# Kernel tuning notes

Measured on AMD Instinct MI355X. Metric: run time of the kernel, lower is better.

Reference implementation:

```python
import jax, jax.numpy as jnp
import numpy as np

EPS = 1e-5
GROUPS = 32


def conv1x1(x, W, b):
    # x: (B,C,T), W: (O,C), b: (O,)
    return jnp.einsum('bct,oc->bot', x, W) + b[None, :, None]


def group_norm(x, gamma, beta):
    B, C, T = x.shape
    xg = x.reshape(B, GROUPS, (C // GROUPS) * T)
    mu = xg.mean(axis=-1, keepdims=True)
    var = xg.var(axis=-1, keepdims=True)
    xn = ((xg - mu) * jax.lax.rsqrt(var + EPS)).reshape(B, C, T)
    return xn * gamma[None, :, None] + beta[None, :, None]


def block(x, W, b, gamma, beta):
    return jax.nn.relu(group_norm(conv1x1(x, W, b), gamma, beta))


def setup_inputs() -> dict:
    key = jax.random.key(0)
    ks = jax.random.split(key, 8)
    B, C, P, T, TF = 4, 512, 512, 2048, 4096
    inp = {
        'feature': jax.random.normal(ks[0], (B, C, T), jnp.float32),
        'frame_level_feature': jax.random.uniform(ks[1], (B, C, TF), jnp.float32),
        # cur_point_conv: conv1x1 C->P + GN(32,P)
        'W1': jax.random.normal(ks[2], (P, C), jnp.float32) / np.sqrt(C),
        'b1': jnp.zeros((P,), jnp.float32),
        'g1': jnp.ones((P,), jnp.float32),
        'be1': jnp.zeros((P,), jnp.float32),
        # lr_conv: conv1x1 C->2P + GN(32,2P)
        'W2': jax.random.normal(ks[3], (2 * P, C), jnp.float32) / np.sqrt(C),
        'b2': jnp.zeros((2 * P,), jnp.float32),
        'g2': jnp.ones((2 * P,), jnp.float32),
        'be2': jnp.zeros((2 * P,), jnp.float32),
        # proposal_conv: conv1x1 4P->C + GN(32,C)
        'W3': jax.random.normal(ks[4], (C, 4 * P), jnp.float32) / np.sqrt(4 * P),
        'b3': jnp.zeros((C,), jnp.float32),
        'g3': jnp.ones((C,), jnp.float32),
        'be3': jnp.zeros((C,), jnp.float32),
    }
    return inp


def reference(feature, frame_level_feature, W1, b1, g1, be1, W2, b2, g2, be2, W3, b3, g3, be3):
    fm_short = block(feature, W1, b1, g1, be1)          # (B,P,T)
    feat = block(feature, W2, b2, g2, be2)              # (B,2P,T)
    t = feature.shape[2]
    # inverse-CDF resampling (uses batch 0 statistics, as original)
    mean_values = frame_level_feature.mean(axis=1)[0]   # (TF,)
    mean_values = mean_values / mean_values.sum()
    cdf = (jnp.cumsum(mean_values) * t).astype(jnp.int32)
    cdf = jnp.minimum(cdf, t - 1)                       # (TF,)
    # exact vectorization of findNearNum loop: first index with minimal |cdf-i|
    targets = jnp.arange(t, dtype=jnp.int32)
    idx = jnp.argmin(jnp.abs(cdf[None, :] - targets[:, None]), axis=1)  # (t,)
    sampled = frame_level_feature[:, :, idx]            # (B,C,t)
    mixed = jnp.concatenate([sampled, feat, fm_short], axis=1)  # (B,4P,t)
    mixed = block(mixed, W3, b3, g3, be3)               # (B,C,t)
    return (mixed, feat)
```

## Files before the change

### kernel.cpp

```cpp
#include <hip/hip_runtime.h>

typedef unsigned short u16;
typedef unsigned int   u32;
typedef __attribute__((ext_vector_type(8))) short short8;
typedef __attribute__((ext_vector_type(4))) float f32x4;

__device__ __forceinline__ float bf2f(u16 v) {
  return __uint_as_float(((u32)v) << 16);
}
__device__ __forceinline__ u16 f2bf(float f) {
  u32 u = __float_as_uint(f);
  u32 r = (u + 0x7FFFu + ((u >> 16) & 1u)) >> 16;
  return (u16)r;
}
__device__ __forceinline__ float relu(float x) { return x < 0.f ? 0.f : x; }

__device__ __forceinline__ void gld16(const void* g, void* l) {
  __builtin_amdgcn_global_load_lds((const __attribute__((address_space(1))) u32*)g,
                                   (__attribute__((address_space(3))) u32*)l, 16, 0, 0);
}

__global__ void colmean_part_kernel(const float* __restrict__ frame,
                                    double* __restrict__ partD) {
  int tf = blockIdx.x * 256 + threadIdx.x;
  int ch = blockIdx.y;
  const float* f0 = frame + tf + (size_t)ch * 64 * 4096;
  double s = 0.0;
  for (int c = 0; c < 64; ++c) s += (double)f0[(size_t)c * 4096];
  partD[ch * 4096 + tf] = s;
}

__global__ void scanD_kernel(const double* __restrict__ partD, int* __restrict__ cdf) {
  __shared__ double part[256];
  __shared__ double base[256];
  __shared__ double Ss;
  int tid = threadIdx.x;
  double loc[16];
  double s = 0.0;
#pragma unroll
  for (int i = 0; i < 16; ++i) {
    int tf = tid * 16 + i;
    double m = 0.0;
#pragma unroll
    for (int ch = 0; ch < 8; ++ch) m += partD[ch * 4096 + tf];
    loc[i] = m / 512.0;
    s += loc[i];
  }
  part[tid] = s;
  __syncthreads();
  if (tid == 0) {
    double t = 0.0;
    for (int i = 0; i < 256; ++i) t += part[i];
    Ss = t;
  }
  __syncthreads();
  double S = Ss;
  s = 0.0;
#pragma unroll
  for (int i = 0; i < 16; ++i) { loc[i] = loc[i] / S; s += loc[i]; }
  part[tid] = s;
  __syncthreads();
  if (tid == 0) {
    double c = 0.0;
    for (int i = 0; i < 256; ++i) { base[i] = c; c += part[i]; }
  }
  __syncthreads();
  double c = base[tid];
#pragma unroll
  for (int i = 0; i < 16; ++i) {
    c += loc[i];
    int iv = (int)(c * 2048.0);
    cdf[tid * 16 + i] = iv < 2047 ? iv : 2047;
  }
}

__global__ void argmin_kernel(const int* __restrict__ cdf, int* __restrict__ idx) {
  __shared__ int sd[256], sj[256];
  int target = blockIdx.x;
  int tid = threadIdx.x;
  int best = 0x7fffffff, bj = 0x7fffffff;
  for (int j = tid; j < 4096; j += 256) {
    int d = cdf[j] - target; d = d < 0 ? -d : d;
    if (d < best) { best = d; bj = j; }
  }
  sd[tid] = best; sj[tid] = bj;
  __syncthreads();
  for (int s = 128; s > 0; s >>= 1) {
    if (tid < s) {
      if (sd[tid+s] < sd[tid] || (sd[tid+s] == sd[tid] && sj[tid+s] < sj[tid])) {
        sd[tid] = sd[tid+s]; sj[tid] = sj[tid+s];
      }
    }
    __syncthreads();
  }
  if (tid == 0) idx[target] = sj[0];
}

__global__ void gatherT_kernel(const float* __restrict__ frame, const int* __restrict__ idx,
                               u16* __restrict__ X3T) {
  __shared__ u16 tile[64][65];
  __shared__ int sidx[64];
  int cb = blockIdx.x * 64, t0 = blockIdx.y * 64, b = blockIdx.z;
  int tid = threadIdx.x;
  if (tid < 64) {
    int it = idx[t0 + tid];
    sidx[tid] = it < 0 ? 0 : (it > 4095 ? 4095 : it);
  }
  __syncthreads();
  const float* fb = frame + (size_t)b * 512 * 4096;
  for (int i = tid; i < 4096; i += 256) {
    int r = i >> 6, tt = i & 63;
    tile[tt][r] = f2bf(fb[(size_t)(cb + r) * 4096 + sidx[tt]]);
  }
  __syncthreads();
  u16* xb = X3T + (size_t)b * 2048 * 2048;
  for (int i = tid; i < 4096; i += 256) {
    int r = i >> 6, cc = i & 63;
    xb[(size_t)(t0 + r) * 2048 + cb + cc] = tile[r][cc];
  }
}

__global__ void transposeCT_kernel(const float* __restrict__ X, u16* __restrict__ XT) {
  __shared__ u16 tile[64][65];
  int cb = blockIdx.x * 64, t0 = blockIdx.y * 64, b = blockIdx.z;
  int tid = threadIdx.x;
  const float* xb = X + (size_t)b * 512 * 2048;
  for (int i = tid; i < 4096; i += 256) {
    int r = i >> 6, tt = i & 63;
    tile[tt][r] = f2bf(xb[(size_t)(cb + r) * 2048 + t0 + tt]);
  }
  __syncthreads();
  u16* xtb = XT + (size_t)b * 2048 * 512;
  for (int i = tid; i < 4096; i += 256) {
    int r = i >> 6, cc = i & 63;
    xtb[(size_t)(t0 + r) * 512 + cb + cc] = tile[r][cc];
  }
}

__global__ void convW_kernel(const float* __restrict__ src, u16* __restrict__ dst, int n) {
  int i = blockIdx.x * 256 + threadIdx.x;
  if (i < n) dst[i] = f2bf(src[i]);
}

__global__ __launch_bounds__(128) void gemm_bt2(
    const u16* __restrict__ A, const u16* __restrict__ Bt,
    const float* __restrict__ bias, float* __restrict__ Y,
    int M, int N, int K)
{
  __shared__ short As[2][2048];
  __shared__ short Bs[2][4096];
  const int tid = threadIdx.x;
  const int lane = tid & 63;
  const int w = tid >> 6;
  const int nt = blockIdx.x, mt = blockIdx.y, bb = blockIdx.z;

  const u16* Ab = A + (size_t)mt * 64 * K;
  const u16* Bb = Bt + ((size_t)bb * N + (size_t)nt * 128) * K;

  const int lm = lane & 15, lq = lane >> 4;

  f32x4 acc[4][4] = {};
  const int nsteps = K >> 5;

  auto stage = [&](int buf, int kt) {
#pragma unroll
    for (int p = 0; p < 2; ++p) {
      int chunk = tid + 128 * p;
      int row = chunk >> 2, ko = (chunk & 3) << 3;
      gld16(Ab + (size_t)row * K + kt + ko, (char*)As[buf] + chunk * 16);
    }
#pragma unroll
    for (int p = 0; p < 4; ++p) {
      int chunk = tid + 128 * p;
      int row = chunk >> 2, ko = (chunk & 3) << 3;
      gld16(Bb + (size_t)row * K + kt + ko, (char*)Bs[buf] + chunk * 16);
    }
  };

  stage(0, 0);
  for (int s = 0; s < nsteps; ++s) {
    int cur = s & 1;
    __syncthreads();
    if (s + 1 < nsteps) stage(cur ^ 1, (s + 1) << 5);
    short8 af[4], bfv[4];
#pragma unroll
    for (int i = 0; i < 4; ++i)
      af[i] = *(const short8*)(As[cur] + ((i * 16 + lm) * 32 + lq * 8));
#pragma unroll
    for (int j = 0; j < 4; ++j)
      bfv[j] = *(const short8*)(Bs[cur] + ((w * 64 + j * 16 + lm) * 32 + lq * 8));
#pragma unroll
    for (int i = 0; i < 4; ++i)
#pragma unroll
      for (int j = 0; j < 4; ++j)
        acc[i][j] = __builtin_amdgcn_mfma_f32_16x16x32_bf16(af[i], bfv[j], acc[i][j], 0, 0, 0);
  }

#pragma unroll
  for (int i = 0; i < 4; ++i) {
    int mbase = mt * 64 + i * 16 + lq * 4;
#pragma unroll
    for (int e = 0; e < 4; ++e) {
      int m = mbase + e;
      float bv = bias[m];
      float* yp = Y + ((size_t)bb * M + m) * N + nt * 128 + w * 64 + lm;
#pragma unroll
      for (int j = 0; j < 4; ++j)
        yp[j * 16] = acc[i][j][e] + bv;
    }
  }
}

__global__ void stats_part_kernel(const float* __restrict__ Y, float* __restrict__ raw,
                                  int C, int cpg) {
  int chunk = blockIdx.x, g = blockIdx.y, b = blockIdx.z, tid = threadIdx.x;
  const float* base = Y + ((size_t)b * C + (size_t)g * cpg) * 2048 + (size_t)chunk * 4096;
  float s = 0.f, ss = 0.f;
#pragma unroll
  for (int i = 0; i < 16; ++i) {
    float v = base[tid + 256 * i];
    s += v; ss += v * v;
  }
  __shared__ float s1[256], s2[256];
  s1[tid] = s; s2[tid] = ss;
  __syncthreads();
  for (int st = 128; st > 0; st >>= 1) {
    if (tid < st) { s1[tid] += s1[tid + st]; s2[tid] += s2[tid + st]; }
    __syncthreads();
  }
  if (tid == 0) {
    atomicAdd(&raw[(b * 32 + g) * 2],     s1[0]);
    atomicAdd(&raw[(b * 32 + g) * 2 + 1], s2[0]);
  }
}

__global__ void stats_fin_kernel(const float* __restrict__ raw, float* __restrict__ stats,
                                 float n) {
  int i = threadIdx.x;
  float mu = raw[i * 2] / n;
  float var = raw[i * 2 + 1] / n - mu * mu;
  stats[i * 2] = mu;
  stats[i * 2 + 1] = 1.0f / sqrtf(var + 1e-5f);
}

__global__ void normT_kernel(const float* __restrict__ Y, const float* __restrict__ stats,
                             const float* __restrict__ gamma, const float* __restrict__ beta,
                             int C, int gShift, u16* __restrict__ X3T, int colBase,
                             float* __restrict__ featOut) {
  __shared__ u16 tile[64][65];
  int b = blockIdx.z, c0 = blockIdx.y * 64, t0 = blockIdx.x * 64;
  const float* yb = Y + (size_t)b * C * 2048;
  for (int i = threadIdx.x; i < 4096; i += 256) {
    int r = i >> 6, cc = i & 63;
    int ch = c0 + r;
    int gI = (b * 32 + (ch >> gShift)) * 2;
    float mu = stats[gI], rs = stats[gI + 1];
    float v = yb[(size_t)ch * 2048 + t0 + cc];
    float o = relu((v - mu) * rs * gamma[ch] + beta[ch]);
    tile[cc][r] = f2bf(o);
    if (featOut) featOut[((size_t)b * C + ch) * 2048 + t0 + cc] = o;
  }
  __syncthreads();
  for (int i = threadIdx.x; i < 4096; i += 256) {
    int r = i >> 6, cc = i & 63;
    X3T[((size_t)b * 2048 + t0 + r) * 2048 + colBase + c0 + cc] = tile[r][cc];
  }
}

__global__ void norm3_kernel(const float* __restrict__ Y, const float* __restrict__ stats,
                             const float* __restrict__ gamma, const float* __restrict__ beta,
                             float* __restrict__ out) {
  int i = blockIdx.x * 256 + threadIdx.x;
  int b = i >> 20;
  int ch = (i >> 11) & 511;
  int gI = (b * 32 + (ch >> 4)) * 2;
  float mu = stats[gI], rs = stats[gI + 1];
  out[i] = relu((Y[i] - mu) * rs * gamma[ch] + beta[ch]);
}

extern "C" void kernel_launch(void* const* d_in, const int* in_sizes, int n_in,
                              void* d_out, int out_size, void* d_ws, size_t ws_size,
                              hipStream_t stream) {
  const float* feature = (const float*)d_in[0];
  const float* frame   = (const float*)d_in[1];
  const float* W1 = (const float*)d_in[2];
  const float* b1 = (const float*)d_in[3];
  const float* g1 = (const float*)d_in[4];
  const float* be1 = (const float*)d_in[5];
  const float* W2 = (const float*)d_in[6];
  const float* b2 = (const float*)d_in[7];
  const float* g2 = (const float*)d_in[8];
  const float* be2 = (const float*)d_in[9];
  const float* W3 = (const float*)d_in[10];
  const float* b3 = (const float*)d_in[11];
  const float* g3 = (const float*)d_in[12];
  const float* be3 = (const float*)d_in[13];

  char* ws = (char*)d_ws;
  u16*    X3T   = (u16*)(ws + 0);
  float*  Y1f   = (float*)(ws + 33554432);
  float*  Y2f   = (float*)(ws + 50331648);
  float*  Y3f   = Y1f;
  u16*    featT = (u16*)(ws + 83886080);
  double* partD = (double*)(ws + 50331648);
  u16*    W1b   = (u16*)(ws + 50331648 + 1048576);
  u16*    W2b   = (u16*)(ws + 33554432);
  u16*    W3b   = (u16*)(ws + 50331648);
  int*    cdf   = (int*)(ws + 92307456);
  int*    idx   = (int*)(ws + 92323840);
  float*  raw1  = (float*)(ws + 92340224);
  float*  raw2  = (float*)(ws + 92341248);
  float*  raw3  = (float*)(ws + 92342272);
  float*  st1   = (float*)(ws + 92343296);
  float*  st2   = (float*)(ws + 92344320);
  float*  st3   = (float*)(ws + 92345344);

  float* outMixed = (float*)d_out;
  float* outFeat  = outMixed + (size_t)4 * 512 * 2048;

  hipMemsetAsync(raw1, 0, 3 * 1024, stream);

  colmean_part_kernel<<<dim3(16, 8), 256, 0, stream>>>(frame, partD);
  scanD_kernel<<<1, 256, 0, stream>>>(partD, cdf);
  argmin_kernel<<<2048, 256, 0, stream>>>(cdf, idx);
  gatherT_kernel<<<dim3(8, 32, 4), 256, 0, stream>>>(frame, idx, X3T);
  transposeCT_kernel<<<dim3(8, 32, 4), 256, 0, stream>>>(feature, featT);

  convW_kernel<<<1024, 256, 0, stream>>>(W1, W1b, 262144);
  gemm_bt2<<<dim3(16, 8, 4), 128, 0, stream>>>(W1b, featT, b1, Y1f, 512, 2048, 512);
  stats_part_kernel<<<dim3(8, 32, 4), 256, 0, stream>>>(Y1f, raw1, 512, 16);
  stats_fin_kernel<<<1, 128, 0, stream>>>(raw1, st1, 32768.f);
  normT_kernel<<<dim3(32, 8, 4), 256, 0, stream>>>(Y1f, st1, g1, be1, 512, 4,
                                                   X3T, 1536, (float*)nullptr);
  convW_kernel<<<2048, 256, 0, stream>>>(W2, W2b, 524288);
  gemm_bt2<<<dim3(16, 16, 4), 128, 0, stream>>>(W2b, featT, b2, Y2f, 1024, 2048, 512);
  stats_part_kernel<<<dim3(16, 32, 4), 256, 0, stream>>>(Y2f, raw2, 1024, 32);
  stats_fin_kernel<<<1, 128, 0, stream>>>(raw2, st2, 65536.f);
  normT_kernel<<<dim3(32, 16, 4), 256, 0, stream>>>(Y2f, st2, g2, be2, 1024, 5,
                                                    X3T, 512, outFeat);
  convW_kernel<<<4096, 256, 0, stream>>>(W3, W3b, 1048576);
  gemm_bt2<<<dim3(16, 8, 4), 128, 0, stream>>>(W3b, X3T, b3, Y3f, 512, 2048, 2048);
  stats_part_kernel<<<dim3(8, 32, 4), 256, 0, stream>>>(Y3f, raw3, 512, 16);
  stats_fin_kernel<<<1, 128, 0, stream>>>(raw3, st3, 32768.f);
  norm3_kernel<<<16384, 256, 0, stream>>>(Y3f, st3, g3, be3, outMixed);
}
```

Baseline: 299.6 us.

## Merge first two conv GEMMs into one launch and split-K the third GEMM

The W1 and W2 weight conversions and their GEMMs are fused into a single launch over a stacked 1536-row weight matrix, so one grid of 1536 blocks covers both. The stats-partial and stats-finalize kernels for these two blocks are also merged, which cuts launch count and fills the GPU better. The K=2048 proposal GEMM is split into two K-halves written to separate partial buffers, doubling its grid to 1024 blocks. Those partials are summed inside the stats and normalization kernels, which adds an extra 16 MB of reads and writes in exchange for more parallelism.

```diff
diff --git a/kernel.cpp b/kernel.cpp
--- a/kernel.cpp
+++ b/kernel.cpp
@@ -137,30 +137,32 @@
   }
 }
 
+__global__ void convW12_kernel(const float* __restrict__ W1, const float* __restrict__ W2,
+                               u16* __restrict__ dst) {
+  int i = blockIdx.x * 256 + threadIdx.x;
+  dst[i] = f2bf(i < 262144 ? W1[i] : W2[i - 262144]);
+}
 __global__ void convW_kernel(const float* __restrict__ src, u16* __restrict__ dst, int n) {
   int i = blockIdx.x * 256 + threadIdx.x;
   if (i < n) dst[i] = f2bf(src[i]);
 }
 
-__global__ __launch_bounds__(128) void gemm_bt2(
+__global__ __launch_bounds__(128) void gemm12_kernel(
     const u16* __restrict__ A, const u16* __restrict__ Bt,
-    const float* __restrict__ bias, float* __restrict__ Y,
-    int M, int N, int K)
+    const float* __restrict__ b1, const float* __restrict__ b2,
+    float* __restrict__ Y)
 {
+  const int K = 512;
   __shared__ short As[2][2048];
   __shared__ short Bs[2][4096];
   const int tid = threadIdx.x;
   const int lane = tid & 63;
   const int w = tid >> 6;
   const int nt = blockIdx.x, mt = blockIdx.y, bb = blockIdx.z;
-
   const u16* Ab = A + (size_t)mt * 64 * K;
-  const u16* Bb = Bt + ((size_t)bb * N + (size_t)nt * 128) * K;
-
+  const u16* Bb = Bt + ((size_t)bb * 2048 + (size_t)nt * 128) * K;
   const int lm = lane & 15, lq = lane >> 4;
-
   f32x4 acc[4][4] = {};
-  const int nsteps = K >> 5;
 
   auto stage = [&](int buf, int kt) {
 #pragma unroll
@@ -178,10 +180,10 @@
   };
 
   stage(0, 0);
-  for (int s = 0; s < nsteps; ++s) {
+  for (int s = 0; s < 16; ++s) {
     int cur = s & 1;
     __syncthreads();
-    if (s + 1 < nsteps) stage(cur ^ 1, (s + 1) << 5);
+    if (s + 1 < 16) stage(cur ^ 1, (s + 1) << 5);
     short8 af[4], bfv[4];
 #pragma unroll
     for (int i = 0; i < 4; ++i)
@@ -195,15 +197,14 @@
       for (int j = 0; j < 4; ++j)
         acc[i][j] = __builtin_amdgcn_mfma_f32_16x16x32_bf16(af[i], bfv[j], acc[i][j], 0, 0, 0);
   }
-
 #pragma unroll
   for (int i = 0; i < 4; ++i) {
     int mbase = mt * 64 + i * 16 + lq * 4;
 #pragma unroll
     for (int e = 0; e < 4; ++e) {
       int m = mbase + e;
-      float bv = bias[m];
-      float* yp = Y + ((size_t)bb * M + m) * N + nt * 128 + w * 64 + lm;
+      float bv = m < 512 ? b1[m] : b2[m - 512];
+      float* yp = Y + ((size_t)bb * 1536 + m) * 2048 + nt * 128 + w * 64 + lm;
 #pragma unroll
       for (int j = 0; j < 4; ++j)
         yp[j * 16] = acc[i][j][e] + bv;
@@ -211,16 +212,81 @@
   }
 }
 
-__global__ void stats_part_kernel(const float* __restrict__ Y, float* __restrict__ raw,
-                                  int C, int cpg) {
-  int chunk = blockIdx.x, g = blockIdx.y, b = blockIdx.z, tid = threadIdx.x;
-  const float* base = Y + ((size_t)b * C + (size_t)g * cpg) * 2048 + (size_t)chunk * 4096;
+__global__ __launch_bounds__(128) void gemm3s_kernel(
+    const u16* __restrict__ A, const u16* __restrict__ Bt,
+    const float* __restrict__ bias, float* __restrict__ Yp)
+{
+  const int K = 2048;
+  __shared__ short As[2][2048];
+  __shared__ short Bs[2][4096];
+  const int tid = threadIdx.x;
+  const int lane = tid & 63;
+  const int w = tid >> 6;
+  const int nt = blockIdx.x, mt = blockIdx.y;
+  const int bb = blockIdx.z >> 1, ks = blockIdx.z & 1;
+  const u16* Ab = A + (size_t)mt * 64 * K + ks * 1024;
+  const u16* Bb = Bt + ((size_t)bb * 2048 + (size_t)nt * 128) * K + ks * 1024;
+  const int lm = lane & 15, lq = lane >> 4;
+  f32x4 acc[4][4] = {};
+
+  auto stage = [&](int buf, int kt) {
+#pragma unroll
+    for (int p = 0; p < 2; ++p) {
+      int chunk = tid + 128 * p;
+      int row = chunk >> 2, ko = (chunk & 3) << 3;
+      gld16(Ab + (size_t)row * K + kt + ko, (char*)As[buf] + chunk * 16);
+    }
+#pragma unroll
+    for (int p = 0; p < 4; ++p) {
+      int chunk = tid + 128 * p;
+      int row = chunk >> 2, ko = (chunk & 3) << 3;
+      gld16(Bb + (size_t)row * K + kt + ko, (char*)Bs[buf] + chunk * 16);
+    }
+  };
+
+  stage(0, 0);
+  for (int s = 0; s < 32; ++s) {
+    int cur = s & 1;
+    __syncthreads();
+    if (s + 1 < 32) stage(cur ^ 1, (s + 1) << 5);
+    short8 af[4], bfv[4];
+#pragma unroll
+    for (int i = 0; i < 4; ++i)
+      af[i] = *(const short8*)(As[cur] + ((i * 16 + lm) * 32 + lq * 8));
+#pragma unroll
+    for (int j = 0; j < 4; ++j)
+      bfv[j] = *(const short8*)(Bs[cur] + ((w * 64 + j * 16 + lm) * 32 + lq * 8));
+#pragma unroll
+    for (int i = 0; i < 4; ++i)
+#pragma unroll
+      for (int j = 0; j < 4; ++j)
+        acc[i][j] = __builtin_amdgcn_mfma_f32_16x16x32_bf16(af[i], bfv[j], acc[i][j], 0, 0, 0);
+  }
+#pragma unroll
+  for (int i = 0; i < 4; ++i) {
+    int mbase = mt * 64 + i * 16 + lq * 4;
+#pragma unroll
+    for (int e = 0; e < 4; ++e) {
+      int m = mbase + e;
+      float bv = ks ? 0.f : bias[m];
+      float* yp = Yp + ((size_t)(ks * 4 + bb) * 512 + m) * 2048 + nt * 128 + w * 64 + lm;
+#pragma unroll
+      for (int j = 0; j < 4; ++j)
+        yp[j * 16] = acc[i][j][e] + bv;
+    }
+  }
+}
+
+__global__ void statsP12_kernel(const float* __restrict__ Y12,
+                                float* __restrict__ raw1, float* __restrict__ raw2) {
+  int chunk = blockIdx.x, gy = blockIdx.y, b = blockIdx.z, tid = threadIdx.x;
+  int cpg, chBase, g; float* raw;
+  if (gy < 32) { if (chunk >= 8) return; cpg = 16; chBase = 0;   g = gy;      raw = raw1; }
+  else         {                         cpg = 32; chBase = 512; g = gy - 32; raw = raw2; }
+  const float* base = Y12 + ((size_t)b * 1536 + chBase + g * cpg) * 2048 + (size_t)chunk * 4096;
   float s = 0.f, ss = 0.f;
 #pragma unroll
-  for (int i = 0; i < 16; ++i) {
-    float v = base[tid + 256 * i];
-    s += v; ss += v * v;
-  }
+  for (int i = 0; i < 16; ++i) { float v = base[tid + 256 * i]; s += v; ss += v * v; }
   __shared__ float s1[256], s2[256];
   s1[tid] = s; s2[tid] = ss;
   __syncthreads();
@@ -234,8 +300,43 @@
   }
 }
 
-__global__ void stats_fin_kernel(const float* __restrict__ raw, float* __restrict__ stats,
-                                 float n) {
+__global__ void stats3p_kernel(const float* __restrict__ Yp, float* __restrict__ raw) {
+  int chunk = blockIdx.x, g = blockIdx.y, b = blockIdx.z, tid = threadIdx.x;
+  const float* base = Yp + ((size_t)b * 512 + g * 16) * 2048 + (size_t)chunk * 4096;
+  float s = 0.f, ss = 0.f;
+#pragma unroll
+  for (int i = 0; i < 16; ++i) {
+    int o = tid + 256 * i;
+    float v = base[o] + base[o + 4194304];
+    s += v; ss += v * v;
+  }
+  __shared__ float s1[256], s2[256];
+  s1[tid] = s; s2[tid] = ss;
+  __syncthreads();
+  for (int st = 128; st > 0; st >>= 1) {
+    if (tid < st) { s1[tid] += s1[tid + st]; s2[tid] += s2[tid + st]; }
+    __syncthreads();
+  }
+  if (tid == 0) {
+    atomicAdd(&raw[(b * 32 + g) * 2],     s1[0]);
+    atomicAdd(&raw[(b * 32 + g) * 2 + 1], s2[0]);
+  }
+}
+
+__global__ void statsFin12_kernel(const float* __restrict__ raw1, const float* __restrict__ raw2,
+                                  float* __restrict__ st1, float* __restrict__ st2) {
+  int i = threadIdx.x;
+  const float* raw = i < 128 ? raw1 : raw2;
+  float* st = i < 128 ? st1 : st2;
+  int j = i & 127;
+  float n = i < 128 ? 32768.f : 65536.f;
+  float mu = raw[j * 2] / n;
+  float var = raw[j * 2 + 1] / n - mu * mu;
+  st[j * 2] = mu;
+  st[j * 2 + 1] = 1.0f / sqrtf(var + 1e-5f);
+}
+__global__ void statsFin_kernel(const float* __restrict__ raw, float* __restrict__ stats,
+                                float n) {
   int i = threadIdx.x;
   float mu = raw[i * 2] / n;
   float var = raw[i * 2 + 1] / n - mu * mu;
@@ -245,11 +346,12 @@
 
 __global__ void normT_kernel(const float* __restrict__ Y, const float* __restrict__ stats,
                              const float* __restrict__ gamma, const float* __restrict__ beta,
-                             int C, int gShift, u16* __restrict__ X3T, int colBase,
+                             int rowsB, int chBase, int C, int gShift,
+                             u16* __restrict__ X3T, int colBase,
                              float* __restrict__ featOut) {
   __shared__ u16 tile[64][65];
   int b = blockIdx.z, c0 = blockIdx.y * 64, t0 = blockIdx.x * 64;
-  const float* yb = Y + (size_t)b * C * 2048;
+  const float* yb = Y + ((size_t)b * rowsB + chBase) * 2048;
   for (int i = threadIdx.x; i < 4096; i += 256) {
     int r = i >> 6, cc = i & 63;
     int ch = c0 + r;
@@ -267,7 +369,7 @@
   }
 }
 
-__global__ void norm3_kernel(const float* __restrict__ Y, const float* __restrict__ stats,
+__global__ void norm3_kernel(const float* __restrict__ Yp, const float* __restrict__ stats,
                              const float* __restrict__ gamma, const float* __restrict__ beta,
                              float* __restrict__ out) {
   int i = blockIdx.x * 256 + threadIdx.x;
@@ -275,7 +377,8 @@
   int ch = (i >> 11) & 511;
   int gI = (b * 32 + (ch >> 4)) * 2;
   float mu = stats[gI], rs = stats[gI + 1];
-  out[i] = relu((Y[i] - mu) * rs * gamma[ch] + beta[ch]);
+  float v = Yp[i] + Yp[i + 4194304];
+  out[i] = relu((v - mu) * rs * gamma[ch] + beta[ch]);
 }
 
 extern "C" void kernel_launch(void* const* d_in, const int* in_sizes, int n_in,
@@ -298,22 +401,20 @@
 
   char* ws = (char*)d_ws;
   u16*    X3T   = (u16*)(ws + 0);
-  float*  Y1f   = (float*)(ws + 33554432);
-  float*  Y2f   = (float*)(ws + 50331648);
-  float*  Y3f   = Y1f;
+  float*  Y12f  = (float*)(ws + 33554432);
+  float*  Y3p   = (float*)(ws + 33554432);
+  u16*    W3b   = (u16*)(ws + 67108864);
+  double* partD = (double*)(ws + 50331648);
   u16*    featT = (u16*)(ws + 83886080);
-  double* partD = (double*)(ws + 50331648);
-  u16*    W1b   = (u16*)(ws + 50331648 + 1048576);
-  u16*    W2b   = (u16*)(ws + 33554432);
-  u16*    W3b   = (u16*)(ws + 50331648);
-  int*    cdf   = (int*)(ws + 92307456);
-  int*    idx   = (int*)(ws + 92323840);
-  float*  raw1  = (float*)(ws + 92340224);
-  float*  raw2  = (float*)(ws + 92341248);
-  float*  raw3  = (float*)(ws + 92342272);
-  float*  st1   = (float*)(ws + 92343296);
-  float*  st2   = (float*)(ws + 92344320);
-  float*  st3   = (float*)(ws + 92345344);
+  u16*    W12b  = (u16*)(ws + 92274688);
+  int*    cdf   = (int*)(ws + 93847552);
+  int*    idx   = (int*)(ws + 93863936);
+  float*  raw1  = (float*)(ws + 93872128);
+  float*  raw2  = (float*)(ws + 93873152);
+  float*  raw3  = (float*)(ws + 93874176);
+  float*  st1   = (float*)(ws + 93875200);
+  float*  st2   = (float*)(ws + 93876224);
+  float*  st3   = (float*)(ws + 93877248);
 
   float* outMixed = (float*)d_out;
   float* outFeat  = outMixed + (size_t)4 * 512 * 2048;
@@ -326,21 +427,17 @@
   gatherT_kernel<<<dim3(8, 32, 4), 256, 0, stream>>>(frame, idx, X3T);
   transposeCT_kernel<<<dim3(8, 32, 4), 256, 0, stream>>>(feature, featT);
 
-  convW_kernel<<<1024, 256, 0, stream>>>(W1, W1b, 262144);
-  gemm_bt2<<<dim3(16, 8, 4), 128, 0, stream>>>(W1b, featT, b1, Y1f, 512, 2048, 512);
-  stats_part_kernel<<<dim3(8, 32, 4), 256, 0, stream>>>(Y1f, raw1, 512, 16);
-  stats_fin_kernel<<<1, 128, 0, stream>>>(raw1, st1, 32768.f);
-  normT_kernel<<<dim3(32, 8, 4), 256, 0, stream>>>(Y1f, st1, g1, be1, 512, 4,
+  convW12_kernel<<<3072, 256, 0, stream>>>(W1, W2, W12b);
+  gemm12_kernel<<<dim3(16, 24, 4), 128, 0, stream>>>(W12b, featT, b1, b2, Y12f);
+  statsP12_kernel<<<dim3(16, 64, 4), 256, 0, stream>>>(Y12f, raw1, raw2);
+  statsFin12_kernel<<<1, 256, 0, stream>>>(raw1, raw2, st1, st2);
+  normT_kernel<<<dim3(32, 8, 4), 256, 0, stream>>>(Y12f, st1, g1, be1, 1536, 0, 512, 4,
                                                    X3T, 1536, (float*)nullptr);
-  convW_kernel<<<2048, 256, 0, stream>>>(W2, W2b, 524288);
-  gemm_bt2<<<dim3(16, 16, 4), 128, 0, stream>>>(W2b, featT, b2, Y2f, 1024, 2048, 512);
-  stats_part_kernel<<<dim3(16, 32, 4), 256, 0, stream>>>(Y2f, raw2, 1024, 32);
-  stats_fin_kernel<<<1, 128, 0, stream>>>(raw2, st2, 65536.f);
-  normT_kernel<<<dim3(32, 16, 4), 256, 0, stream>>>(Y2f, st2, g2, be2, 1024, 5,
+  normT_kernel<<<dim3(32, 16, 4), 256, 0, stream>>>(Y12f, st2, g2, be2, 1536, 512, 1024, 5,
                                                     X3T, 512, outFeat);
   convW_kernel<<<4096, 256, 0, stream>>>(W3, W3b, 1048576);
-  gemm_bt2<<<dim3(16, 8, 4), 128, 0, stream>>>(W3b, X3T, b3, Y3f, 512, 2048, 2048);
-  stats_part_kernel<<<dim3(8, 32, 4), 256, 0, stream>>>(Y3f, raw3, 512, 16);
-  stats_fin_kernel<<<1, 128, 0, stream>>>(raw3, st3, 32768.f);
-  norm3_kernel<<<16384, 256, 0, stream>>>(Y3f, st3, g3, be3, outMixed);
-}
+  gemm3s_kernel<<<dim3(16, 8, 8), 128, 0, stream>>>(W3b, X3T, b3, Y3p);
+  stats3p_kernel<<<dim3(8, 32, 4), 256, 0, stream>>>(Y3p, raw3);
+  statsFin_kernel<<<1, 128, 0, stream>>>(raw3, st3, 32768.f);
+  norm3_kernel<<<16384, 256, 0, stream>>>(Y3p, st3, g3, be3, outMixed);
+}
```

Measured after the change: 285.5 us. -4.7%, faster.
